# Performance work log

Hardware: AMD Instinct MI355X
Metric: run time of the kernel (lower is better)

## Reference

```python
import jax, jax.numpy as jnp
import numpy as np

N_TOK = 40   # sentence length n
BS = 8       # batch size
D = 256      # span-rep / MLP input size
H = 256      # MLP hidden size
NEG = -1e30  # log-zero


def setup_inputs() -> dict:
    key = jax.random.key(0)
    k0, k1, k2, k3 = jax.random.split(key, 4)
    enc = jax.random.normal(k0, (N_TOK + 1, BS, D), jnp.float32)  # boundary encodings
    W1 = jax.random.normal(k1, (2 * D, H), jnp.float32) * 0.05    # MLP layer 1 (concat(left,right) -> h)
    b1 = jnp.zeros((H,), jnp.float32)
    W2 = jax.random.normal(k2, (H, 2), jnp.float32) * 0.05        # MLP layer 2 (h -> 2 ops: straight/inverted)
    b2 = jnp.zeros((2,), jnp.float32)
    lengths = jax.random.randint(k3, (BS,), 2, N_TOK + 1)         # per-example sentence lengths in [2, n]
    return {"enc": enc, "W1": W1, "b1": b1, "W2": W2, "b2": b2, "lengths": lengths}


def _inside(enc, W1, b1, W2, b2, lengths):
    n1, bs, d = enc.shape
    n = n1 - 1
    # span_rep.get_span(i,j) -> boundary difference enc[j] - enc[i]; [n+1,n+1,bs,d]
    span = enc[None] - enc[:, None]
    # MLP on concat(left, right): split W1 so hidden[i,j,k] = relu(L[i,j] + R[j,k] + b1)
    Lh = jnp.einsum('ijbd,dh->ijbh', span, W1[:d])
    Rh = jnp.einsum('ijbd,dh->ijbh', span, W1[d:])
    hidden = jax.nn.relu(Lh[:, :, None] + Rh[None] + b1)          # [n+1,n+1,n+1,bs,h]
    S = jnp.einsum('ijkbh,ho->ijkbo', hidden, W2) + b2            # decision scores [i,j,k,bs,2]
    # CKY inside recursion over span widths
    B = jnp.full((n1, n1, bs), jnp.float32(NEG))
    idx = jnp.arange(n)
    B = B.at[idx, idx + 1].set(0.0)                               # beta[i,i+1] = 0
    for w in range(2, n + 1):
        m = n - w + 1
        i_idx = jnp.arange(m)
        s = jnp.arange(1, w)
        j_idx = i_idx[:, None] + s[None, :]                       # [m, w-1] split points
        k_idx = i_idx + w
        sc = S[i_idx[:, None], j_idx, k_idx[:, None]]             # [m, w-1, bs, 2]
        bsum = B[i_idx[:, None], j_idx] + B[j_idx, k_idx[:, None]]  # beta[i,j]+beta[j,k], [m, w-1, bs]
        gamma = sc + bsum[..., None]
        new_beta = jax.scipy.special.logsumexp(gamma, axis=(1, 3))  # [m, bs]
        B = B.at[i_idx, k_idx].set(new_beta)
    # partition[b] = beta[0, lengths[b]][b]
    return B[0, lengths, jnp.arange(bs)]


def reference(enc, W1, b1, W2, b2, lengths):
    return _inside(enc, W1, b1, W2, b2, lengths)
```

## Files before the change

### kernel.cpp

```cpp
#include <hip/hip_runtime.h>
#include <math.h>

#define N_TOK 40
#define N1    41
#define BS    8
#define DD    256
#define HH    256
#define NTRI  10660
#define NPAIR 780
#define NPTASK (NPAIR * BS)
#define ROWF  (BS * N1 * HH)
#define MNEG  (-1e38f)
#define DPB   256

__global__ __launch_bounds__(256) void k_proj(
    const float* __restrict__ enc, const float* __restrict__ W1,
    const float* __restrict__ b1v,
    float* __restrict__ P, float* __restrict__ Qb, float* __restrict__ Dd)
{
    const int blk  = blockIdx.x;
    const int t    = blk >> 2;
    const int hq   = blk & 3;
    const int tid  = threadIdx.x;
    const int lane = tid & 63;
    const int pr   = tid >> 6;

    __shared__ float w1T[512][64];
    __shared__ float e[BS][DD];

    #pragma unroll 8
    for (int r = pr; r < 512; r += 4)
        w1T[r][lane] = W1[(r << 8) + (hq << 6) + lane];
    for (int x = tid; x < BS * DD; x += 256)
        e[x >> 8][x & 255] = enc[(t * BS + (x >> 8)) * DD + (x & 255)];
    __syncthreads();

    const int h  = (hq << 6) + lane;
    const int bA = 2 * pr, bB = 2 * pr + 1;

    float a0 = 0.f, c0 = 0.f, a1 = 0.f, c1 = 0.f;
    #pragma unroll 8
    for (int d = 0; d < DD; ++d) {
        float wp = w1T[d][lane];
        float wq = w1T[256 + d][lane];
        float e0 = e[bA][d];
        float e1 = e[bB][d];
        a0 = fmaf(e0, wp, a0); c0 = fmaf(e0, wq, c0);
        a1 = fmaf(e1, wp, a1); c1 = fmaf(e1, wq, c1);
    }

    const float bb = b1v[h];
    const int iA = ((bA * N1) + t) * HH + h;
    const int iB = ((bB * N1) + t) * HH + h;
    P[iA]  = a0;          P[iB]  = a1;
    Qb[iA] = c0 + bb;     Qb[iB] = c1 + bb;
    Dd[iA] = a0 - c0;     Dd[iB] = a1 - c1;
}

__global__ __launch_bounds__(256) void k_score(
    const float* __restrict__ P, const float* __restrict__ Qb,
    const float* __restrict__ Dd, const float* __restrict__ W2,
    const float* __restrict__ b2, float* __restrict__ S)
{
    const int task = blockIdx.x * 4 + (threadIdx.x >> 6);
    const int lane = threadIdx.x & 63;
    const int js   = lane >> 4;
    const int t    = lane & 15;

    const int p = task >> 3;
    const int b = task & 7;

    int c = (int)((sqrtf(8.f * (float)p + 1.f) - 1.f) * 0.5f);
    while ((c + 1) * (c + 2) / 2 <= p) ++c;
    while (c * (c + 1) / 2 > p) --c;
    const int w    = 40 - c;
    const int i    = p - c * (c + 1) / 2;
    const int k    = i + w;
    const int nj   = w - 1;
    const int n2   = w - 2;
    const int base = n2 * (n2 + 1) * (119 - 2 * n2) / 6;

    const float4* Pr  = (const float4*)(P  + ((b * N1 + i) << 8)) + t * 4;
    const float4* Qr  = (const float4*)(Qb + ((b * N1 + k) << 8)) + t * 4;
    const float4* W2r = (const float4*)(W2) + t * 8;

    float4 pp[4], qq[4], wa[4], wb[4];
    #pragma unroll
    for (int q = 0; q < 4; ++q) {
        pp[q] = Pr[q]; qq[q] = Qr[q];
        wa[q] = W2r[q * 2]; wb[q] = W2r[q * 2 + 1];
    }
    const float bb0 = b2[0], bb1 = b2[1];
    float* Sout = S + b * NTRI + base + i * nj;

    for (int jp = js; jp < nj; jp += 4) {
        const float4* Drow =
            (const float4*)(Dd + ((b * N1 + i + 1 + jp) << 8)) + t * 4;
        float s0 = 0.f, s1 = 0.f;
        #pragma unroll
        for (int q = 0; q < 4; ++q) {
            float4 dd = Drow[q];
            float r0 = fmaxf(dd.x + qq[q].x - pp[q].x, 0.f);
            float r1 = fmaxf(dd.y + qq[q].y - pp[q].y, 0.f);
            float r2 = fmaxf(dd.z + qq[q].z - pp[q].z, 0.f);
            float r3 = fmaxf(dd.w + qq[q].w - pp[q].w, 0.f);
            s0 = fmaf(r0, wa[q].x, s0); s1 = fmaf(r0, wa[q].y, s1);
            s0 = fmaf(r1, wa[q].z, s0); s1 = fmaf(r1, wa[q].w, s1);
            s0 = fmaf(r2, wb[q].x, s0); s1 = fmaf(r2, wb[q].y, s1);
            s0 = fmaf(r3, wb[q].z, s0); s1 = fmaf(r3, wb[q].w, s1);
        }
        #pragma unroll
        for (int d = 1; d < 16; d <<= 1) {
            s0 += __shfl_xor(s0, d);
            s1 += __shfl_xor(s1, d);
        }
        if (t == 0) {
            float S0 = s0 + bb0, S1 = s1 + bb1;
            Sout[jp] = fmaxf(S0, S1) + log1pf(__expf(-fabsf(S0 - S1)));
        }
    }
}

__device__ __forceinline__ int tri_base(int i) { return (i * (81 - i)) >> 1; }
#define BIDX(i, j) (tri_base(i) + ((j) - (i) - 1))

constexpr int soff(int W) {
    int s = 0;
    for (int v = 2; v < W; ++v) s += (N1 - v) * (v - 1);
    return s;
}
constexpr int pick_T(int m, int nj) {
    int T = 1;
    while (T < 16 && m * (T * 2) <= DPB && T < nj) T *= 2;
    return T;
}

template<int W>
__device__ __forceinline__ void dp_step(float* __restrict__ Btri,
                                        const float* __restrict__ Sl, int tid)
{
    constexpr int m    = N1 - W;
    constexpr int nj   = W - 1;
    constexpr int T    = pick_T(m, nj);
    constexpr int CH   = (nj + T - 1) / T;
    constexpr int base = soff(W);

    if (tid < m * T) {
        const int i = tid / T;
        const int h = tid % T;
        const int k = i + W;

        float g[CH];
        #pragma unroll
        for (int q = 0; q < CH; ++q) {
            int jp = h + q * T;
            bool live = (q < CH - 1) || (jp < nj);
            int jj = live ? jp : 0;
            float v = Sl[base + i * nj + jj]
                    + Btri[BIDX(i, i + 1 + jj)]
                    + Btri[BIDX(i + 1 + jj, k)];
            g[q] = live ? v : MNEG;
        }
        float mx = g[0];
        #pragma unroll
        for (int q = 1; q < CH; ++q) mx = fmaxf(mx, g[q]);
        float s = 0.f;
        #pragma unroll
        for (int q = 0; q < CH; ++q) s += __expf(g[q] - mx);
        #pragma unroll
        for (int d = 1; d < T; d <<= 1) {
            float mo = __shfl_xor(mx, d);
            float so = __shfl_xor(s, d);
            float nm = fmaxf(mx, mo);
            s = s * __expf(mx - nm) + so * __expf(mo - nm);
            mx = nm;
        }
        if (h == 0)
            Btri[BIDX(i, k)] = mx + __logf(s);
    }
    __syncthreads();
}

template<int W>
__device__ __forceinline__ void dp_from(float* __restrict__ Btri,
                                        const float* __restrict__ Sl, int tid)
{
    dp_step<W>(Btri, Sl, tid);
    if constexpr (W + 1 <= N_TOK) dp_from<W + 1>(Btri, Sl, tid);
}

__global__ __launch_bounds__(DPB) void k_dp(
    const float* __restrict__ Sg, const int* __restrict__ lengths,
    float* __restrict__ out)
{
    __shared__ __align__(16) float Sl[NTRI];
    __shared__ float Btri[820];
    const int tid = threadIdx.x;
    const int b   = blockIdx.x;

    const float4* src = (const float4*)(Sg + b * NTRI);
    float4* dst = (float4*)Sl;
    for (int x = tid; x < NTRI / 4; x += DPB) dst[x] = src[x];
    if (tid < N_TOK) Btri[tri_base(tid)] = 0.f;
    __syncthreads();

    dp_from<2>(Btri, Sl, tid);

    if (tid == 0) {
        int L = lengths[b];
        out[b] = Btri[BIDX(0, L)];
    }
}

extern "C" void kernel_launch(void* const* d_in, const int* in_sizes, int n_in,
                              void* d_out, int out_size, void* d_ws, size_t ws_size,
                              hipStream_t stream)
{
    const float* enc = (const float*)d_in[0];
    const float* W1  = (const float*)d_in[1];
    const float* b1  = (const float*)d_in[2];
    const float* W2  = (const float*)d_in[3];
    const float* b2  = (const float*)d_in[4];
    const int* lengths = (const int*)d_in[5];

    float* ws = (float*)d_ws;
    float* P  = ws;
    float* Qb = ws + ROWF;
    float* Dd = ws + 2 * ROWF;
    float* S  = ws + 3 * ROWF;

    k_proj<<<dim3(164), dim3(256), 0, stream>>>(enc, W1, b1, P, Qb, Dd);
    k_score<<<dim3(NPTASK / 4), dim3(256), 0, stream>>>(P, Qb, Dd, W2, b2, S);
    k_dp<<<dim3(BS), dim3(DPB), 0, stream>>>(S, lengths, (float*)d_out);
}
```

Before: 115.0 us.

## Fuse score and DP kernels with per-batch last-block atomic handoff

Merges the score kernel and the CKY DP kernel into one launch. Each batch gets 49 blocks of 1024 threads that compute scores, then signal a per-batch global atomic counter. The last block (g == GPB-1) spins until all blocks of its batch arrive, then runs the DP in shared memory and resets the counter. This removes one kernel launch and its inter-kernel gap, at the risk of a deadlock if the waiting block is resident while other blocks cannot be scheduled. The DP block size also grows to 1024 threads, but the tid < m*T guard leaves the extra threads idle.

```diff
diff --git a/kernel.cpp b/kernel.cpp
--- a/kernel.cpp
+++ b/kernel.cpp
@@ -8,10 +8,14 @@
 #define HH    256
 #define NTRI  10660
 #define NPAIR 780
-#define NPTASK (NPAIR * BS)
 #define ROWF  (BS * N1 * HH)
 #define MNEG  (-1e38f)
 #define DPB   256
+#define GPB   49
+#define NBF   (BS * GPB)
+#define THR   1024
+
+__device__ unsigned long long g_sync[BS][512];
 
 __global__ __launch_bounds__(256) void k_proj(
     const float* __restrict__ enc, const float* __restrict__ W1,
@@ -57,70 +61,6 @@
     Dd[iA] = a0 - c0;     Dd[iB] = a1 - c1;
 }
 
-__global__ __launch_bounds__(256) void k_score(
-    const float* __restrict__ P, const float* __restrict__ Qb,
-    const float* __restrict__ Dd, const float* __restrict__ W2,
-    const float* __restrict__ b2, float* __restrict__ S)
-{
-    const int task = blockIdx.x * 4 + (threadIdx.x >> 6);
-    const int lane = threadIdx.x & 63;
-    const int js   = lane >> 4;
-    const int t    = lane & 15;
-
-    const int p = task >> 3;
-    const int b = task & 7;
-
-    int c = (int)((sqrtf(8.f * (float)p + 1.f) - 1.f) * 0.5f);
-    while ((c + 1) * (c + 2) / 2 <= p) ++c;
-    while (c * (c + 1) / 2 > p) --c;
-    const int w    = 40 - c;
-    const int i    = p - c * (c + 1) / 2;
-    const int k    = i + w;
-    const int nj   = w - 1;
-    const int n2   = w - 2;
-    const int base = n2 * (n2 + 1) * (119 - 2 * n2) / 6;
-
-    const float4* Pr  = (const float4*)(P  + ((b * N1 + i) << 8)) + t * 4;
-    const float4* Qr  = (const float4*)(Qb + ((b * N1 + k) << 8)) + t * 4;
-    const float4* W2r = (const float4*)(W2) + t * 8;
-
-    float4 pp[4], qq[4], wa[4], wb[4];
-    #pragma unroll
-    for (int q = 0; q < 4; ++q) {
-        pp[q] = Pr[q]; qq[q] = Qr[q];
-        wa[q] = W2r[q * 2]; wb[q] = W2r[q * 2 + 1];
-    }
-    const float bb0 = b2[0], bb1 = b2[1];
-    float* Sout = S + b * NTRI + base + i * nj;
-
-    for (int jp = js; jp < nj; jp += 4) {
-        const float4* Drow =
-            (const float4*)(Dd + ((b * N1 + i + 1 + jp) << 8)) + t * 4;
-        float s0 = 0.f, s1 = 0.f;
-        #pragma unroll
-        for (int q = 0; q < 4; ++q) {
-            float4 dd = Drow[q];
-            float r0 = fmaxf(dd.x + qq[q].x - pp[q].x, 0.f);
-            float r1 = fmaxf(dd.y + qq[q].y - pp[q].y, 0.f);
-            float r2 = fmaxf(dd.z + qq[q].z - pp[q].z, 0.f);
-            float r3 = fmaxf(dd.w + qq[q].w - pp[q].w, 0.f);
-            s0 = fmaf(r0, wa[q].x, s0); s1 = fmaf(r0, wa[q].y, s1);
-            s0 = fmaf(r1, wa[q].z, s0); s1 = fmaf(r1, wa[q].w, s1);
-            s0 = fmaf(r2, wb[q].x, s0); s1 = fmaf(r2, wb[q].y, s1);
-            s0 = fmaf(r3, wb[q].z, s0); s1 = fmaf(r3, wb[q].w, s1);
-        }
-        #pragma unroll
-        for (int d = 1; d < 16; d <<= 1) {
-            s0 += __shfl_xor(s0, d);
-            s1 += __shfl_xor(s1, d);
-        }
-        if (t == 0) {
-            float S0 = s0 + bb0, S1 = s1 + bb1;
-            Sout[jp] = fmaxf(S0, S1) + log1pf(__expf(-fabsf(S0 - S1)));
-        }
-    }
-}
-
 __device__ __forceinline__ int tri_base(int i) { return (i * (81 - i)) >> 1; }
 #define BIDX(i, j) (tri_base(i) + ((j) - (i) - 1))
 
@@ -189,27 +129,113 @@
     if constexpr (W + 1 <= N_TOK) dp_from<W + 1>(Btri, Sl, tid);
 }
 
-__global__ __launch_bounds__(DPB) void k_dp(
-    const float* __restrict__ Sg, const int* __restrict__ lengths,
-    float* __restrict__ out)
-{
-    __shared__ __align__(16) float Sl[NTRI];
-    __shared__ float Btri[820];
+__global__ __launch_bounds__(THR) void k_sdp(
+    const float* __restrict__ P, const float* __restrict__ Qb,
+    const float* __restrict__ Dd, const float* __restrict__ W2,
+    const float* __restrict__ b2, const int* __restrict__ lengths,
+    float* __restrict__ S, float* __restrict__ out)
+{
     const int tid = threadIdx.x;
-    const int b   = blockIdx.x;
-
-    const float4* src = (const float4*)(Sg + b * NTRI);
-    float4* dst = (float4*)Sl;
-    for (int x = tid; x < NTRI / 4; x += DPB) dst[x] = src[x];
-    if (tid < N_TOK) Btri[tri_base(tid)] = 0.f;
-    __syncthreads();
-
-    dp_from<2>(Btri, Sl, tid);
-
+    const int blk = blockIdx.x;
+    const int b   = blk / GPB;
+    const int g   = blk - b * GPB;
+
+    __shared__ __align__(16) struct { float Sl[NTRI]; float Btri[820]; } sh;
+
+    {
+        const int widx = tid >> 6;
+        const int lane = tid & 63;
+        const int js   = lane >> 4;
+        const int t    = lane & 15;
+        const int p    = g * 16 + widx;
+
+        if (p < NPAIR) {
+            int c = (int)((sqrtf(8.f * (float)p + 1.f) - 1.f) * 0.5f);
+            while ((c + 1) * (c + 2) / 2 <= p) ++c;
+            while (c * (c + 1) / 2 > p) --c;
+            const int w    = 40 - c;
+            const int i    = p - c * (c + 1) / 2;
+            const int k    = i + w;
+            const int nj   = w - 1;
+            const int n2   = w - 2;
+            const int base = n2 * (n2 + 1) * (119 - 2 * n2) / 6;
+
+            const float4* Pr  = (const float4*)(P  + ((b * N1 + i) << 8)) + t * 4;
+            const float4* Qr  = (const float4*)(Qb + ((b * N1 + k) << 8)) + t * 4;
+            const float4* W2r = (const float4*)(W2) + t * 8;
+
+            float4 pp[4], qq[4], wa[4], wb[4];
+            #pragma unroll
+            for (int q = 0; q < 4; ++q) {
+                pp[q] = Pr[q]; qq[q] = Qr[q];
+                wa[q] = W2r[q * 2]; wb[q] = W2r[q * 2 + 1];
+            }
+            const float bb0 = b2[0], bb1 = b2[1];
+            float* Sout = S + b * NTRI + base + i * nj;
+
+            for (int jp = js; jp < nj; jp += 4) {
+                const float4* Drow =
+                    (const float4*)(Dd + ((b * N1 + i + 1 + jp) << 8)) + t * 4;
+                float s0 = 0.f, s1 = 0.f;
+                #pragma unroll
+                for (int q = 0; q < 4; ++q) {
+                    float4 dd = Drow[q];
+                    float r0 = fmaxf(dd.x + qq[q].x - pp[q].x, 0.f);
+                    float r1 = fmaxf(dd.y + qq[q].y - pp[q].y, 0.f);
+                    float r2 = fmaxf(dd.z + qq[q].z - pp[q].z, 0.f);
+                    float r3 = fmaxf(dd.w + qq[q].w - pp[q].w, 0.f);
+                    s0 = fmaf(r0, wa[q].x, s0); s1 = fmaf(r0, wa[q].y, s1);
+                    s0 = fmaf(r1, wa[q].z, s0); s1 = fmaf(r1, wa[q].w, s1);
+                    s0 = fmaf(r2, wb[q].x, s0); s1 = fmaf(r2, wb[q].y, s1);
+                    s0 = fmaf(r3, wb[q].z, s0); s1 = fmaf(r3, wb[q].w, s1);
+                }
+                #pragma unroll
+                for (int d = 1; d < 16; d <<= 1) {
+                    s0 += __shfl_xor(s0, d);
+                    s1 += __shfl_xor(s1, d);
+                }
+                if (t == 0) {
+                    float S0 = s0 + bb0, S1 = s1 + bb1;
+                    Sout[jp] = fmaxf(S0, S1) + log1pf(__expf(-fabsf(S0 - S1)));
+                }
+            }
+        }
+    }
+
+    __syncthreads();
     if (tid == 0) {
-        int L = lengths[b];
-        out[b] = Btri[BIDX(0, L)];
-    }
+        __threadfence();
+        __hip_atomic_fetch_add(&g_sync[b][0], 1ull, __ATOMIC_RELEASE,
+                               __HIP_MEMORY_SCOPE_AGENT);
+    }
+    if (g != GPB - 1) return;
+
+    if (tid == 0) {
+        while (__hip_atomic_load(&g_sync[b][0], __ATOMIC_RELAXED,
+                                 __HIP_MEMORY_SCOPE_AGENT) < (unsigned long long)GPB)
+            __builtin_amdgcn_s_sleep(16);
+        __threadfence();
+    }
+    __syncthreads();
+
+    {
+        const float4* src = (const float4*)(S + b * NTRI);
+        float4* dst = (float4*)sh.Sl;
+        for (int x = tid; x < NTRI / 4; x += THR) dst[x] = src[x];
+        if (tid < N_TOK) sh.Btri[tri_base(tid)] = 0.f;
+        __syncthreads();
+
+        dp_from<2>(sh.Btri, sh.Sl, tid);
+
+        if (tid == 0) {
+            int L = lengths[b];
+            out[b] = sh.Btri[BIDX(0, L)];
+        }
+    }
+
+    if (tid == 0)
+        __hip_atomic_store(&g_sync[b][0], 0ull, __ATOMIC_RELAXED,
+                           __HIP_MEMORY_SCOPE_AGENT);
 }
 
 extern "C" void kernel_launch(void* const* d_in, const int* in_sizes, int n_in,
@@ -230,6 +256,6 @@
     float* S  = ws + 3 * ROWF;
 
     k_proj<<<dim3(164), dim3(256), 0, stream>>>(enc, W1, b1, P, Qb, Dd);
-    k_score<<<dim3(NPTASK / 4), dim3(256), 0, stream>>>(P, Qb, Dd, W2, b2, S);
-    k_dp<<<dim3(BS), dim3(DPB), 0, stream>>>(S, lengths, (float*)d_out);
-}
+    k_sdp<<<dim3(NBF), dim3(THR), 0, stream>>>(P, Qb, Dd, W2, b2, lengths,
+                                               S, (float*)d_out);
+}
```

Result: slower. 129.3 us (+12.4%).
